# Kernel optimization log

Measured on AMD Instinct MI355X. Metric: run time of the kernel, lower is better.

Reference implementation:

```python
import jax, jax.numpy as jnp
import numpy as np

N_NODES = 20000


def _segment_softmax(alpha, dst, num_nodes):
    # numerically-stable softmax over edges grouped by destination node
    m = jax.ops.segment_max(alpha, dst, num_segments=num_nodes)
    m = jnp.where(jnp.isfinite(m), m, 0.0)
    a = jnp.exp(alpha - m[dst])
    denom = jax.ops.segment_sum(a, dst, num_segments=num_nodes)
    return a / denom[dst]


def mgcn_conv(x, src, dst, edge_type, basis, att, weight, root, bias, num_nodes):
    # x: [N, in], basis: [B, in, out], att: [R, B], weight: [R, out=in]
    x_i = x[dst]                                   # [E, in] target feats
    x_j = x[src]                                   # [E, in] source feats
    # per-edge attention logit: sum_d x_i[d] * w_r[d] * x_j[d]
    alpha = jnp.sum(x_i * weight[edge_type] * x_j, axis=1)   # [E]
    alpha = _segment_softmax(alpha, dst, num_nodes)          # [E]
    # basis-decomposed per-edge transform: x_j @ (att_r . basis)
    t = jnp.einsum('ei,bio->ebo', x_j, basis)                # [E, B, out]
    msg = jnp.einsum('ebo,eb->eo', t, att[edge_type])        # [E, out]
    msg = msg * alpha[:, None]
    out = jax.ops.segment_sum(msg, dst, num_segments=num_nodes)  # [N, out]
    return out + x @ root + bias


def setup_inputs() -> dict:
    key = jax.random.key(0)
    ks = jax.random.split(key, 16)
    E, D, R, B, N = 32768, 128, 474, 64, N_NODES
    s = 0.05
    return {
        'entity': jnp.arange(N, dtype=jnp.int64) if jax.config.jax_enable_x64 else jnp.arange(N, dtype=jnp.int32),
        'edge_index': jax.random.randint(ks[0], (2, E), 0, N, dtype=jnp.int32),
        'edge_type': jax.random.randint(ks[1], (E,), 0, R, dtype=jnp.int32),
        'emb_table': jax.random.normal(ks[2], (N, D), dtype=jnp.float32),
        'basis1': jax.random.normal(ks[3], (B, D, D), dtype=jnp.float32) * s,
        'att1': jax.random.normal(ks[4], (R, B), dtype=jnp.float32) * s,
        'weight1': jax.random.normal(ks[5], (R, D), dtype=jnp.float32) * s,
        'root1': jax.random.normal(ks[6], (D, D), dtype=jnp.float32) * s,
        'bias1': jnp.zeros((D,), dtype=jnp.float32),
        'basis2': jax.random.normal(ks[7], (B, D, D), dtype=jnp.float32) * s,
        'att2': jax.random.normal(ks[8], (R, B), dtype=jnp.float32) * s,
        'weight2': jax.random.normal(ks[9], (R, D), dtype=jnp.float32) * s,
        'root2': jax.random.normal(ks[10], (D, D), dtype=jnp.float32) * s,
        'bias2': jnp.zeros((D,), dtype=jnp.float32),
    }


def reference(entity, edge_index, edge_type, emb_table,
              basis1, att1, weight1, root1, bias1,
              basis2, att2, weight2, root2, bias2):
    src, dst = edge_index[0], edge_index[1]   # PyG: (source j, target i)
    x = emb_table[entity]                     # embedding lookup
    h = jax.nn.relu(mgcn_conv(x, src, dst, edge_type, basis1, att1,
                              weight1, root1, bias1, N_NODES))
    # dropout is identity at inference
    out = mgcn_conv(h, src, dst, edge_type, basis2, att2,
                    weight2, root2, bias2, N_NODES)
    return out
```

## Files before the change

kernel.cpp:

```cpp
#include <hip/hip_runtime.h>
#include <hip/hip_bf16.h>

#define N_NODES 20000
#define N_EDGES 32768
#define DIM 128
#define N_REL 474
#define N_BASIS 64
#define TILE_E 64
#define MAXCH (N_EDGES / TILE_E + N_REL)
#define WSTRIDE 260

typedef __bf16 bf16x8 __attribute__((ext_vector_type(8)));
typedef float f32x4 __attribute__((ext_vector_type(4)));

__device__ __forceinline__ unsigned short f2b(float f) {
    unsigned u = __float_as_uint(f);
    unsigned r = (u + 0x7FFFu + ((u >> 16) & 1u)) >> 16;
    return (unsigned short)r;
}
__device__ __forceinline__ float b2f(unsigned short s) {
    return __uint_as_float(((unsigned)s) << 16);
}
__device__ __forceinline__ __bf16 u2b(unsigned short u) {
    union { unsigned short u; __bf16 b; } c; c.u = u; return c.b;
}

__global__ __launch_bounds__(256) void prep_kernel(const float4* __restrict__ emb,
                                                   const int* __restrict__ entity,
                                                   const int* __restrict__ etype,
                                                   ushort4* __restrict__ xb4,
                                                   float4* __restrict__ zreg, int zcount4,
                                                   int* __restrict__ cnt) {
    int gtid = blockIdx.x * 256 + threadIdx.x;
    int gsz = gridDim.x * 256;
    int total4 = N_NODES * DIM / 4;
    for (int i = gtid; i < total4; i += gsz) {
        int n = i >> 5, rem = i & 31;
        float4 v = emb[(size_t)entity[n] * 32 + rem];
        ushort4 s;
        s.x = f2b(v.x); s.y = f2b(v.y); s.z = f2b(v.z); s.w = f2b(v.w);
        xb4[i] = s;
    }
    for (int e = gtid; e < N_EDGES; e += gsz) atomicAdd(&cnt[etype[e]], 1);
    float4 z = make_float4(0.f, 0.f, 0.f, 0.f);
    for (int i = gtid; i < zcount4; i += gsz) zreg[i] = z;
}

__global__ void scanr_kernel(const int* __restrict__ cnt, int* __restrict__ offs,
                             int* __restrict__ cursor, int* __restrict__ chunk_r,
                             int* __restrict__ chunk_o, int* __restrict__ nchunks,
                             int R, int E) {
    __shared__ int s[512];
    int t = threadIdx.x;
    int v = (t < R) ? cnt[t] : 0;
    s[t] = v;
    __syncthreads();
    for (int d = 1; d < 512; d <<= 1) {
        int add = (t >= d) ? s[t - d] : 0;
        __syncthreads();
        s[t] += add;
        __syncthreads();
    }
    int excl = s[t] - v;
    if (t < R) { offs[t] = excl; cursor[t] = excl; }
    if (t == 0) offs[R] = E;
    int nc = (v + TILE_E - 1) / TILE_E;
    if (t < R && nc > 0) {
        int b = atomicAdd(nchunks, nc);
        for (int c = 0; c < nc; c++) { chunk_r[b + c] = t; chunk_o[b + c] = excl + c * TILE_E; }
    }
}

__global__ __launch_bounds__(256) void scatlogit_kernel(const unsigned short* __restrict__ xb,
                                                        const float* __restrict__ w,
                                                        const int* __restrict__ src,
                                                        const int* __restrict__ dst,
                                                        const int* __restrict__ et,
                                                        int* __restrict__ cursor,
                                                        int* __restrict__ eids,
                                                        float* __restrict__ alpha,
                                                        float* __restrict__ den, int E) {
    int wid = (blockIdx.x * 256 + threadIdx.x) >> 6;
    int lane = threadIdx.x & 63;
    if (wid >= E) return;
    int s = src[wid], d = dst[wid], r = et[wid];
    if (lane == 0) {
        int p = atomicAdd(&cursor[r], 1);
        eids[p] = wid;
    }
    unsigned ax = ((const unsigned*)(xb + (size_t)s * DIM))[lane];
    unsigned bx = ((const unsigned*)(xb + (size_t)d * DIM))[lane];
    float2 wv = ((const float2*)(w + (size_t)r * DIM))[lane];
    float v = b2f((unsigned short)(ax & 0xFFFF)) * wv.x * b2f((unsigned short)(bx & 0xFFFF))
            + b2f((unsigned short)(ax >> 16)) * wv.y * b2f((unsigned short)(bx >> 16));
    for (int off = 32; off > 0; off >>= 1) v += __shfl_xor(v, off, 64);
    if (lane == 0) {
        float a = expf(v);
        alpha[wid] = a;
        atomicAdd(&den[d], a);
    }
}

__global__ __launch_bounds__(256) void logitexp_kernel(const unsigned short* __restrict__ xb,
                                                       const float* __restrict__ w,
                                                       const int* __restrict__ src,
                                                       const int* __restrict__ dst,
                                                       const int* __restrict__ et,
                                                       float* __restrict__ alpha,
                                                       float* __restrict__ den, int E) {
    int wid = (blockIdx.x * 256 + threadIdx.x) >> 6;
    int lane = threadIdx.x & 63;
    if (wid >= E) return;
    int s = src[wid], d = dst[wid], r = et[wid];
    unsigned ax = ((const unsigned*)(xb + (size_t)s * DIM))[lane];
    unsigned bx = ((const unsigned*)(xb + (size_t)d * DIM))[lane];
    float2 wv = ((const float2*)(w + (size_t)r * DIM))[lane];
    float v = b2f((unsigned short)(ax & 0xFFFF)) * wv.x * b2f((unsigned short)(bx & 0xFFFF))
            + b2f((unsigned short)(ax >> 16)) * wv.y * b2f((unsigned short)(bx >> 16));
    for (int off = 32; off > 0; off >>= 1) v += __shfl_xor(v, off, 64);
    if (lane == 0) {
        float a = expf(v);
        alpha[wid] = a;
        atomicAdd(&den[d], a);
    }
}

__global__ __launch_bounds__(256) void wmix_kernel(const float* __restrict__ att1,
                                                   const float* __restrict__ basis1,
                                                   unsigned short* __restrict__ W1,
                                                   const float* __restrict__ att2,
                                                   const float* __restrict__ basis2,
                                                   unsigned short* __restrict__ W2, int R) {
    const float* att   = (blockIdx.y < 8) ? att1 : att2;
    const float* basis = (blockIdx.y < 8) ? basis1 : basis2;
    unsigned short* W  = (blockIdx.y < 8) ? W1 : W2;
    int io0 = blockIdx.x * 256;
    int r0 = (blockIdx.y & 7) * 64;
    __shared__ unsigned short bt[64 * WSTRIDE];
    int t = threadIdx.x;
#pragma unroll
    for (int p = 0; p < 16; p++) {
        int c = t + 256 * p;
        int k = c >> 6, of = c & 63;
        float4 v = *(const float4*)(basis + (size_t)k * (DIM * DIM) + io0 + of * 4);
        ushort4 s;
        s.x = f2b(v.x); s.y = f2b(v.y); s.z = f2b(v.z); s.w = f2b(v.w);
        *(ushort4*)&bt[k * WSTRIDE + of * 4] = s;
    }
    __syncthreads();

    int w = t >> 6, l = t & 63, n = l & 15, q = l >> 4;
    f32x4 acc[4][4] = {};
#pragma unroll
    for (int kb = 0; kb < 2; kb++) {
        int kbase = kb * 32 + q * 8;
        bf16x8 a[4];
#pragma unroll
        for (int rt = 0; rt < 4; rt++) {
            int rm = min(r0 + rt * 16 + n, R - 1);
            const float* ap = att + (size_t)rm * N_BASIS + kbase;
#pragma unroll
            for (int j = 0; j < 8; j++) a[rt][j] = u2b(f2b(ap[j]));
        }
#pragma unroll
        for (int c = 0; c < 4; c++) {
            int ob = w * 64 + c * 16 + n;
            bf16x8 b;
#pragma unroll
            for (int j = 0; j < 8; j++) b[j] = u2b(bt[(kbase + j) * WSTRIDE + ob]);
#pragma unroll
            for (int rt = 0; rt < 4; rt++)
                acc[rt][c] = __builtin_amdgcn_mfma_f32_16x16x32_bf16(a[rt], b, acc[rt][c], 0, 0, 0);
        }
    }
#pragma unroll
    for (int rt = 0; rt < 4; rt++) {
#pragma unroll
        for (int c = 0; c < 4; c++) {
            int col = io0 + w * 64 + c * 16 + n;
#pragma unroll
            for (int rg = 0; rg < 4; rg++) {
                int r = r0 + rt * 16 + q * 4 + rg;
                if (r < R) W[(size_t)r * (DIM * DIM) + col] = f2b(acc[rt][c][rg]);
            }
        }
    }
}

__global__ __launch_bounds__(256) void msg_kernel(const unsigned short* __restrict__ xb,
                                                  const unsigned short* __restrict__ W,
                                                  const int* __restrict__ chunk_r,
                                                  const int* __restrict__ chunk_off,
                                                  const int* __restrict__ nchunks,
                                                  const int* __restrict__ eids,
                                                  const int* __restrict__ offs,
                                                  const int* __restrict__ src,
                                                  const int* __restrict__ dst,
                                                  const float* __restrict__ ae,
                                                  const float* __restrict__ denom,
                                                  float* __restrict__ outacc) {
    if ((int)blockIdx.x >= *nchunks) return;
    int r = chunk_r[blockIdx.x];
    int base = chunk_off[blockIdx.x];
    int nE = min(TILE_E, offs[r + 1] - base);
    const unsigned short* Wr = W + (size_t)r * (DIM * DIM);

    __shared__ unsigned short wt[128 * 136];
    __shared__ unsigned short xjf[8192];
    __shared__ float scf[TILE_E];
    __shared__ int sdd[TILE_E];

    int t = threadIdx.x;
    if (t < TILE_E) {
        if (t < nE) {
            int e = eids[base + t];
            int d_ = dst[e];
            sdd[t] = d_;
            scf[t] = ae[e] / denom[d_];
        } else { sdd[t] = 0; scf[t] = 0.f; }
    }
#pragma unroll
    for (int p = 0; p < 4; p++) {
        int c = t + 256 * p;
        int g = c >> 6;
        int rt = g >> 2, kb = g & 3;
        int q = (c >> 4) & 3, m = c & 15;
        int e = rt * 16 + m;
        int oct = kb * 4 + q;
        int4 v = make_int4(0, 0, 0, 0);
        if (e < nE)
            v = *(const int4*)(xb + (size_t)src[eids[base + e]] * DIM + oct * 8);
        *(int4*)&xjf[c * 8] = v;
    }
#pragma unroll
    for (int p = 0; p < 8; p++) {
        int c = t + 256 * p;
        int k = c >> 4, oct = c & 15;
        int4 v = *(const int4*)(Wr + k * DIM + oct * 8);
        *(int4*)&wt[k * 136 + oct * 8] = v;
    }
    __syncthreads();

    int w = t >> 6, l = t & 63, n = l & 15, q = l >> 4;
    f32x4 acc[2][4] = {};
#pragma unroll
    for (int kb = 0; kb < 4; kb++) {
        bf16x8 a[4];
#pragma unroll
        for (int rt = 0; rt < 4; rt++) a[rt] = *(const bf16x8*)&xjf[((rt * 4 + kb) * 64 + l) * 8];
        int kbase = kb * 32 + q * 8;
#pragma unroll
        for (int c = 0; c < 2; c++) {
            int ob = (w * 2 + c) * 16 + n;
            bf16x8 b;
#pragma unroll
            for (int j = 0; j < 8; j++) b[j] = u2b(wt[(kbase + j) * 136 + ob]);
#pragma unroll
            for (int rt = 0; rt < 4; rt++)
                acc[c][rt] = __builtin_amdgcn_mfma_f32_16x16x32_bf16(a[rt], b, acc[c][rt], 0, 0, 0);
        }
    }
#pragma unroll
    for (int c = 0; c < 2; c++) {
        int col = (w * 2 + c) * 16 + n;
#pragma unroll
        for (int rt = 0; rt < 4; rt++) {
#pragma unroll
            for (int rg = 0; rg < 4; rg++) {
                int e = rt * 16 + q * 4 + rg;
                if (e < nE)
                    atomicAdd(&outacc[(size_t)sdd[e] * DIM + col], scf[e] * acc[c][rt][rg]);
            }
        }
    }
}

__global__ __launch_bounds__(256) void root_kernel(const unsigned short* __restrict__ xb,
                                                   const float* __restrict__ rootM,
                                                   const float* __restrict__ bias,
                                                   const float* __restrict__ accbuf,
                                                   unsigned short* __restrict__ outb,
                                                   float* __restrict__ outf,
                                                   int mode, int N) {
    int n0 = blockIdx.x * 64;
    __shared__ unsigned short wt[128 * 136];
    __shared__ unsigned short xrf[8192];
    int t = threadIdx.x;
#pragma unroll
    for (int p = 0; p < 4; p++) {
        int c = t + 256 * p;
        int g = c >> 6;
        int rt = g >> 2, kb = g & 3;
        int q = (c >> 4) & 3, m = c & 15;
        int row = n0 + rt * 16 + m;
        int oct = kb * 4 + q;
        int4 v = make_int4(0, 0, 0, 0);
        if (row < N) v = *(const int4*)(xb + (size_t)row * DIM + oct * 8);
        *(int4*)&xrf[c * 8] = v;
    }
#pragma unroll
    for (int p = 0; p < 16; p++) {
        int c = t + 256 * p;
        int k = c >> 5, of = c & 31;
        float4 v = *(const float4*)(rootM + k * DIM + of * 4);
        ushort4 s;
        s.x = f2b(v.x); s.y = f2b(v.y); s.z = f2b(v.z); s.w = f2b(v.w);
        *(ushort4*)&wt[k * 136 + of * 4] = s;
    }
    __syncthreads();

    int w = t >> 6, l = t & 63, n = l & 15, q = l >> 4;
    f32x4 acc[2][4] = {};
#pragma unroll
    for (int kb = 0; kb < 4; kb++) {
        bf16x8 a[4];
#pragma unroll
        for (int rt = 0; rt < 4; rt++) a[rt] = *(const bf16x8*)&xrf[((rt * 4 + kb) * 64 + l) * 8];
        int kbase = kb * 32 + q * 8;
#pragma unroll
        for (int c = 0; c < 2; c++) {
            int ob = (w * 2 + c) * 16 + n;
            bf16x8 b;
#pragma unroll
            for (int j = 0; j < 8; j++) b[j] = u2b(wt[(kbase + j) * 136 + ob]);
#pragma unroll
            for (int rt = 0; rt < 4; rt++)
                acc[c][rt] = __builtin_amdgcn_mfma_f32_16x16x32_bf16(a[rt], b, acc[c][rt], 0, 0, 0);
        }
    }
#pragma unroll
    for (int c = 0; c < 2; c++) {
        int col = (w * 2 + c) * 16 + n;
        float bo = bias[col];
#pragma unroll
        for (int rt = 0; rt < 4; rt++) {
#pragma unroll
            for (int rg = 0; rg < 4; rg++) {
                int row = n0 + rt * 16 + q * 4 + rg;
                if (row < N) {
                    float v = accbuf[(size_t)row * DIM + col] + acc[c][rt][rg] + bo;
                    if (mode) {
                        outb[(size_t)row * DIM + col] = f2b(fmaxf(v, 0.f));
                    } else {
                        outf[(size_t)row * DIM + col] = v;
                    }
                }
            }
        }
    }
}

extern "C" void kernel_launch(void* const* d_in, const int* in_sizes, int n_in,
                              void* d_out, int out_size, void* d_ws, size_t ws_size,
                              hipStream_t stream) {
    const int N = N_NODES, E = N_EDGES, R = N_REL;

    const int* entity = (const int*)d_in[0];
    const int* eidx   = (const int*)d_in[1];
    const int* src    = eidx;
    const int* dst    = eidx + E;
    const int* etype  = (const int*)d_in[2];
    const float* emb  = (const float*)d_in[3];
    const float* basis1 = (const float*)d_in[4];
    const float* att1   = (const float*)d_in[5];
    const float* w1     = (const float*)d_in[6];
    const float* root1  = (const float*)d_in[7];
    const float* bias1  = (const float*)d_in[8];
    const float* basis2 = (const float*)d_in[9];
    const float* att2   = (const float*)d_in[10];
    const float* w2     = (const float*)d_in[11];
    const float* root2  = (const float*)d_in[12];
    const float* bias2  = (const float*)d_in[13];
    float* out = (float*)d_out;

    size_t off = 0;
    auto alloc = [&](size_t bytes) -> void* {
        void* p = (char*)d_ws + off;
        off += (bytes + 255) & ~(size_t)255;
        return p;
    };
    unsigned short* W1 = (unsigned short*)alloc((size_t)R * DIM * DIM * 2);
    unsigned short* W2 = (unsigned short*)alloc((size_t)R * DIM * DIM * 2);
    unsigned short* xb = (unsigned short*)alloc((size_t)N * DIM * 2);
    unsigned short* hb = (unsigned short*)alloc((size_t)N * DIM * 2);
    float* zreg   = (float*)alloc((size_t)(2 * N * DIM + 2 * N) * 4);
    float* acc1   = zreg;
    float* acc2   = zreg + (size_t)N * DIM;
    float* denom1 = zreg + (size_t)2 * N * DIM;
    float* denom2 = denom1 + N;
    float* alpha  = (float*)alloc((size_t)E * 4);
    int* meta     = (int*)alloc((size_t)(R + 1) * 4);
    int* cnt      = meta;
    int* nchunks  = meta + R;
    int* offs     = (int*)alloc((size_t)(R + 1) * 4);
    int* cursor   = (int*)alloc((size_t)R * 4);
    int* eids     = (int*)alloc((size_t)E * 4);
    int* chunk_r  = (int*)alloc((size_t)MAXCH * 4);
    int* chunk_o  = (int*)alloc((size_t)MAXCH * 4);

    int zcount4 = (2 * N * DIM + 2 * N) / 4;

    hipMemsetAsync(meta, 0, (size_t)(R + 1) * 4, stream);
    prep_kernel<<<2048, 256, 0, stream>>>((const float4*)emb, entity, etype,
                                          (ushort4*)xb, (float4*)zreg, zcount4, cnt);
    scanr_kernel<<<1, 512, 0, stream>>>(cnt, offs, cursor, chunk_r, chunk_o, nchunks, R, E);
    wmix_kernel<<<dim3(64, 16), 256, 0, stream>>>(att1, basis1, W1, att2, basis2, W2, R);

    scatlogit_kernel<<<E / 4, 256, 0, stream>>>(xb, w1, src, dst, etype, cursor, eids,
                                                alpha, denom1, E);
    msg_kernel<<<MAXCH, 256, 0, stream>>>(xb, W1, chunk_r, chunk_o, nchunks,
                                          eids, offs, src, dst, alpha, denom1, acc1);
    root_kernel<<<(N + 63) / 64, 256, 0, stream>>>(xb, root1, bias1, acc1, hb, nullptr, 1, N);

    logitexp_kernel<<<E / 4, 256, 0, stream>>>(hb, w2, src, dst, etype, alpha, denom2, E);
    msg_kernel<<<MAXCH, 256, 0, stream>>>(hb, W2, chunk_r, chunk_o, nchunks,
                                          eids, offs, src, dst, alpha, denom2, acc2);
    root_kernel<<<(N + 63) / 64, 256, 0, stream>>>(hb, root2, bias2, acc2, nullptr, out, 0, N);
}
```

Baseline: 249.6 us.

## Fuse weight-mix into prep kernel and use per-block shared histograms

Merges the basis-mixing MFMA kernel and the embedding/zeroing prep kernel into one launch, with 1024 blocks doing the weight mix and 1024 doing conversion and zeroing. Relation counting moves from global atomics to 16 shared-memory partial histograms that the scan kernel sums. The scan now allocates chunks through a shared-memory counter, which removes the memset launch and its global atomics. The cost is that prep blocks now carry the mix kernel's shared-memory footprint, which can lower occupancy for the memory-bound half.

```diff
diff --git a/kernel.cpp b/kernel.cpp
--- a/kernel.cpp
+++ b/kernel.cpp
@@ -9,6 +9,8 @@
 #define TILE_E 64
 #define MAXCH (N_EDGES / TILE_E + N_REL)
 #define WSTRIDE 260
+#define HIST_BLKS 16
+#define EDGES_PER_HIST (N_EDGES / HIST_BLKS)
 
 typedef __bf16 bf16x8 __attribute__((ext_vector_type(8)));
 typedef float f32x4 __attribute__((ext_vector_type(4)));
@@ -25,35 +27,114 @@
     union { unsigned short u; __bf16 b; } c; c.u = u; return c.b;
 }
 
-__global__ __launch_bounds__(256) void prep_kernel(const float4* __restrict__ emb,
-                                                   const int* __restrict__ entity,
-                                                   const int* __restrict__ etype,
-                                                   ushort4* __restrict__ xb4,
-                                                   float4* __restrict__ zreg, int zcount4,
-                                                   int* __restrict__ cnt) {
-    int gtid = blockIdx.x * 256 + threadIdx.x;
-    int gsz = gridDim.x * 256;
-    int total4 = N_NODES * DIM / 4;
-    for (int i = gtid; i < total4; i += gsz) {
-        int n = i >> 5, rem = i & 31;
-        float4 v = emb[(size_t)entity[n] * 32 + rem];
-        ushort4 s;
-        s.x = f2b(v.x); s.y = f2b(v.y); s.z = f2b(v.z); s.w = f2b(v.w);
-        xb4[i] = s;
-    }
-    for (int e = gtid; e < N_EDGES; e += gsz) atomicAdd(&cnt[etype[e]], 1);
-    float4 z = make_float4(0.f, 0.f, 0.f, 0.f);
-    for (int i = gtid; i < zcount4; i += gsz) zreg[i] = z;
-}
-
-__global__ void scanr_kernel(const int* __restrict__ cnt, int* __restrict__ offs,
+__global__ __launch_bounds__(256) void prepmix_kernel(const float4* __restrict__ emb,
+                                                      const int* __restrict__ entity,
+                                                      const int* __restrict__ etype,
+                                                      ushort4* __restrict__ xb4,
+                                                      float4* __restrict__ zreg, int zcount4,
+                                                      int* __restrict__ partial,
+                                                      const float* __restrict__ att1,
+                                                      const float* __restrict__ basis1,
+                                                      unsigned short* __restrict__ W1,
+                                                      const float* __restrict__ att2,
+                                                      const float* __restrict__ basis2,
+                                                      unsigned short* __restrict__ W2) {
+    __shared__ __align__(16) unsigned short bt[64 * WSTRIDE];
+    int t = threadIdx.x;
+    if (blockIdx.x < 1024) {
+        int wi = blockIdx.x;
+        const float* att   = (wi >= 512) ? att2 : att1;
+        const float* basis = (wi >= 512) ? basis2 : basis1;
+        unsigned short* W  = (wi >= 512) ? W2 : W1;
+        int io0 = (wi & 63) * 256;
+        int r0 = ((wi >> 6) & 7) * 64;
+#pragma unroll
+        for (int p = 0; p < 16; p++) {
+            int c = t + 256 * p;
+            int k = c >> 6, of = c & 63;
+            float4 v = *(const float4*)(basis + (size_t)k * (DIM * DIM) + io0 + of * 4);
+            ushort4 s;
+            s.x = f2b(v.x); s.y = f2b(v.y); s.z = f2b(v.z); s.w = f2b(v.w);
+            *(ushort4*)&bt[k * WSTRIDE + of * 4] = s;
+        }
+        __syncthreads();
+
+        int w = t >> 6, l = t & 63, n = l & 15, q = l >> 4;
+        f32x4 acc[4][4] = {};
+#pragma unroll
+        for (int kb = 0; kb < 2; kb++) {
+            int kbase = kb * 32 + q * 8;
+            bf16x8 a[4];
+#pragma unroll
+            for (int rt = 0; rt < 4; rt++) {
+                int rm = min(r0 + rt * 16 + n, N_REL - 1);
+                const float* ap = att + (size_t)rm * N_BASIS + kbase;
+#pragma unroll
+                for (int j = 0; j < 8; j++) a[rt][j] = u2b(f2b(ap[j]));
+            }
+#pragma unroll
+            for (int c = 0; c < 4; c++) {
+                int ob = w * 64 + c * 16 + n;
+                bf16x8 b;
+#pragma unroll
+                for (int j = 0; j < 8; j++) b[j] = u2b(bt[(kbase + j) * WSTRIDE + ob]);
+#pragma unroll
+                for (int rt = 0; rt < 4; rt++)
+                    acc[rt][c] = __builtin_amdgcn_mfma_f32_16x16x32_bf16(a[rt], b, acc[rt][c], 0, 0, 0);
+            }
+        }
+#pragma unroll
+        for (int rt = 0; rt < 4; rt++) {
+#pragma unroll
+            for (int c = 0; c < 4; c++) {
+                int col = io0 + w * 64 + c * 16 + n;
+#pragma unroll
+                for (int rg = 0; rg < 4; rg++) {
+                    int r = r0 + rt * 16 + q * 4 + rg;
+                    if (r < N_REL) W[(size_t)r * (DIM * DIM) + col] = f2b(acc[rt][c][rg]);
+                }
+            }
+        }
+    } else {
+        int pb = blockIdx.x - 1024;
+        int gtid = pb * 256 + t;
+        int gsz = 1024 * 256;
+        int total4 = N_NODES * DIM / 4;
+        for (int i = gtid; i < total4; i += gsz) {
+            int n = i >> 5, rem = i & 31;
+            float4 v = emb[(size_t)entity[n] * 32 + rem];
+            ushort4 s;
+            s.x = f2b(v.x); s.y = f2b(v.y); s.z = f2b(v.z); s.w = f2b(v.w);
+            xb4[i] = s;
+        }
+        float4 z = make_float4(0.f, 0.f, 0.f, 0.f);
+        for (int i = gtid; i < zcount4; i += gsz) zreg[i] = z;
+        if (pb < HIST_BLKS) {
+            int* ih = (int*)bt;
+            for (int i = t; i < N_REL; i += 256) ih[i] = 0;
+            __syncthreads();
+            int e0 = pb * EDGES_PER_HIST;
+            for (int e = e0 + t; e < e0 + EDGES_PER_HIST; e += 256)
+                atomicAdd(&ih[etype[e]], 1);
+            __syncthreads();
+            for (int i = t; i < N_REL; i += 256) partial[pb * N_REL + i] = ih[i];
+        }
+    }
+}
+
+__global__ void scanr_kernel(const int* __restrict__ partial, int* __restrict__ offs,
                              int* __restrict__ cursor, int* __restrict__ chunk_r,
-                             int* __restrict__ chunk_o, int* __restrict__ nchunks,
-                             int R, int E) {
+                             int* __restrict__ chunk_o, int* __restrict__ nchunks) {
     __shared__ int s[512];
+    __shared__ int lnc;
     int t = threadIdx.x;
-    int v = (t < R) ? cnt[t] : 0;
+    int v = 0;
+    if (t < N_REL) {
+#pragma unroll
+        for (int k = 0; k < HIST_BLKS; k++) v += partial[k * N_REL + t];
+    }
     s[t] = v;
+    if (t == 0) lnc = 0;
     __syncthreads();
     for (int d = 1; d < 512; d <<= 1) {
         int add = (t >= d) ? s[t - d] : 0;
@@ -62,13 +143,15 @@
         __syncthreads();
     }
     int excl = s[t] - v;
-    if (t < R) { offs[t] = excl; cursor[t] = excl; }
-    if (t == 0) offs[R] = E;
-    int nc = (v + TILE_E - 1) / TILE_E;
-    if (t < R && nc > 0) {
-        int b = atomicAdd(nchunks, nc);
-        for (int c = 0; c < nc; c++) { chunk_r[b + c] = t; chunk_o[b + c] = excl + c * TILE_E; }
-    }
+    if (t < N_REL) { offs[t] = excl; cursor[t] = excl; }
+    if (t == 0) offs[N_REL] = N_EDGES;
+    if (t < N_REL && v > 0) {
+        int nc = (v + TILE_E - 1) / TILE_E;
+        int cb = atomicAdd(&lnc, nc);
+        for (int c = 0; c < nc; c++) { chunk_r[cb + c] = t; chunk_o[cb + c] = excl + c * TILE_E; }
+    }
+    __syncthreads();
+    if (t == 0) *nchunks = lnc;
 }
 
 __global__ __launch_bounds__(256) void scatlogit_kernel(const unsigned short* __restrict__ xb,
@@ -125,68 +208,6 @@
     }
 }
 
-__global__ __launch_bounds__(256) void wmix_kernel(const float* __restrict__ att1,
-                                                   const float* __restrict__ basis1,
-                                                   unsigned short* __restrict__ W1,
-                                                   const float* __restrict__ att2,
-                                                   const float* __restrict__ basis2,
-                                                   unsigned short* __restrict__ W2, int R) {
-    const float* att   = (blockIdx.y < 8) ? att1 : att2;
-    const float* basis = (blockIdx.y < 8) ? basis1 : basis2;
-    unsigned short* W  = (blockIdx.y < 8) ? W1 : W2;
-    int io0 = blockIdx.x * 256;
-    int r0 = (blockIdx.y & 7) * 64;
-    __shared__ unsigned short bt[64 * WSTRIDE];
-    int t = threadIdx.x;
-#pragma unroll
-    for (int p = 0; p < 16; p++) {
-        int c = t + 256 * p;
-        int k = c >> 6, of = c & 63;
-        float4 v = *(const float4*)(basis + (size_t)k * (DIM * DIM) + io0 + of * 4);
-        ushort4 s;
-        s.x = f2b(v.x); s.y = f2b(v.y); s.z = f2b(v.z); s.w = f2b(v.w);
-        *(ushort4*)&bt[k * WSTRIDE + of * 4] = s;
-    }
-    __syncthreads();
-
-    int w = t >> 6, l = t & 63, n = l & 15, q = l >> 4;
-    f32x4 acc[4][4] = {};
-#pragma unroll
-    for (int kb = 0; kb < 2; kb++) {
-        int kbase = kb * 32 + q * 8;
-        bf16x8 a[4];
-#pragma unroll
-        for (int rt = 0; rt < 4; rt++) {
-            int rm = min(r0 + rt * 16 + n, R - 1);
-            const float* ap = att + (size_t)rm * N_BASIS + kbase;
-#pragma unroll
-            for (int j = 0; j < 8; j++) a[rt][j] = u2b(f2b(ap[j]));
-        }
-#pragma unroll
-        for (int c = 0; c < 4; c++) {
-            int ob = w * 64 + c * 16 + n;
-            bf16x8 b;
-#pragma unroll
-            for (int j = 0; j < 8; j++) b[j] = u2b(bt[(kbase + j) * WSTRIDE + ob]);
-#pragma unroll
-            for (int rt = 0; rt < 4; rt++)
-                acc[rt][c] = __builtin_amdgcn_mfma_f32_16x16x32_bf16(a[rt], b, acc[rt][c], 0, 0, 0);
-        }
-    }
-#pragma unroll
-    for (int rt = 0; rt < 4; rt++) {
-#pragma unroll
-        for (int c = 0; c < 4; c++) {
-            int col = io0 + w * 64 + c * 16 + n;
-#pragma unroll
-            for (int rg = 0; rg < 4; rg++) {
-                int r = r0 + rt * 16 + q * 4 + rg;
-                if (r < R) W[(size_t)r * (DIM * DIM) + col] = f2b(acc[rt][c][rg]);
-            }
-        }
-    }
-}
-
 __global__ __launch_bounds__(256) void msg_kernel(const unsigned short* __restrict__ xb,
                                                   const unsigned short* __restrict__ W,
                                                   const int* __restrict__ chunk_r,
@@ -389,9 +410,8 @@
     float* denom1 = zreg + (size_t)2 * N * DIM;
     float* denom2 = denom1 + N;
     float* alpha  = (float*)alloc((size_t)E * 4);
-    int* meta     = (int*)alloc((size_t)(R + 1) * 4);
-    int* cnt      = meta;
-    int* nchunks  = meta + R;
+    int* partial  = (int*)alloc((size_t)HIST_BLKS * R * 4);
+    int* nchunks  = (int*)alloc(256);
     int* offs     = (int*)alloc((size_t)(R + 1) * 4);
     int* cursor   = (int*)alloc((size_t)R * 4);
     int* eids     = (int*)alloc((size_t)E * 4);
@@ -400,11 +420,10 @@
 
     int zcount4 = (2 * N * DIM + 2 * N) / 4;
 
-    hipMemsetAsync(meta, 0, (size_t)(R + 1) * 4, stream);
-    prep_kernel<<<2048, 256, 0, stream>>>((const float4*)emb, entity, etype,
-                                          (ushort4*)xb, (float4*)zreg, zcount4, cnt);
-    scanr_kernel<<<1, 512, 0, stream>>>(cnt, offs, cursor, chunk_r, chunk_o, nchunks, R, E);
-    wmix_kernel<<<dim3(64, 16), 256, 0, stream>>>(att1, basis1, W1, att2, basis2, W2, R);
+    prepmix_kernel<<<2048, 256, 0, stream>>>((const float4*)emb, entity, etype,
+                                             (ushort4*)xb, (float4*)zreg, zcount4, partial,
+                                             att1, basis1, W1, att2, basis2, W2);
+    scanr_kernel<<<1, 512, 0, stream>>>(partial, offs, cursor, chunk_r, chunk_o, nchunks);
 
     scatlogit_kernel<<<E / 4, 256, 0, stream>>>(xb, w1, src, dst, etype, cursor, eids,
                                                 alpha, denom1, E);
```

New measurement: 230.9 us. 1.08x faster.
